# Kernel optimization log

Measured on AMD Instinct MI355X. Metric: run time of the kernel, lower is better.

## Reference

```python
import jax, jax.numpy as jnp
import numpy as np

N = 50000       # nodes
E = 1600000     # edges (avg degree 32)
D = 128         # in = hidden = out channels
H = 4           # attention heads


def setup_inputs() -> dict:
    key = jax.random.key(0)
    ks = jax.random.split(key, 9)
    s = 1.0 / np.sqrt(D)  # ~kaiming-scale linear weights
    return {
        "x": jax.random.normal(ks[0], (N, D), jnp.float32),
        "Wk": jax.random.normal(ks[1], (D, D), jnp.float32) * s,
        "bk": jnp.zeros((D,), jnp.float32),
        "Wq": jax.random.normal(ks[2], (D, D), jnp.float32) * s,
        "bq": jnp.zeros((D,), jnp.float32),
        "Wv": jax.random.normal(ks[3], (D, D), jnp.float32) * s,
        "bv": jnp.zeros((D,), jnp.float32),
        "src": jax.random.randint(ks[4], (E,), 0, N, dtype=jnp.int32),
        "dst": jax.random.randint(ks[5], (E,), 0, N, dtype=jnp.int32),
    }


def reference(x, Wk, bk, Wq, bq, Wv, bv, src, dst):
    n = x.shape[0]
    heads = H
    dk = Wk.shape[0] // heads
    dv = Wv.shape[0] // heads
    # Dense projections (near-roofline GEMMs)
    k = (x @ Wk.T + bk).reshape(n, heads, dk)
    q = (x @ Wq.T + bq).reshape(n, heads, dk)
    v = (x @ Wv.T + bv).reshape(n, heads, dv)
    # u_dot_v: per-edge per-head dot product (NO 1/sqrt(dk) scaling in source)
    scores = jnp.einsum('ehd,ehd->eh', k[src], q[dst])  # [E,H]
    # edge_softmax: softmax over incoming edges of each destination node
    m = jax.ops.segment_max(scores, dst, num_segments=n)        # [N,H]
    p = jnp.exp(scores - m[dst])                                 # [E,H]
    denom = jax.ops.segment_sum(p, dst, num_segments=n)         # [N,H]
    alpha = p / denom[dst]                                       # [E,H]
    # u_mul_e + sum: weighted scatter-aggregation of source values
    res = jax.ops.segment_sum(v[src] * alpha[:, :, None], dst, num_segments=n)  # [N,H,dv]
    # original: view(batch_size, -1, out_channels) with batch_size = N -> [N,1,out]
    return res.reshape(n, 1, heads * dv)
```

## Files before the change

kernel.cpp:

```cpp
#include <hip/hip_runtime.h>
#include <hip/hip_bf16.h>
#include <hip/hip_fp16.h>

#define NN 50000
#define NE 1600000
#define DD 128
#define HH 4
#define BSH2 5
#define NBKT2 1563
#define NBP2 2048
#define CAP 1408
#define PCHUNK 8192
#define NPB 196
#define GEMMB 782
#define MIDB (GEMMB + NPB)

typedef __attribute__((ext_vector_type(8))) short short8;
typedef __attribute__((ext_vector_type(4))) float floatx4;
typedef __attribute__((ext_vector_type(2))) _Float16 h2;

__device__ inline h2 as_h2(unsigned u) {
    union { unsigned u; h2 h; } c; c.u = u; return c.h;
}

__device__ inline float dot4(h2 a01, h2 a23, h2 b01, h2 b23) {
#if defined(__has_builtin) && __has_builtin(__builtin_amdgcn_fdot2)
    return __builtin_amdgcn_fdot2(a01, b01, __builtin_amdgcn_fdot2(a23, b23, 0.f, false), false);
#else
    return (float)a01.x * (float)b01.x + (float)a01.y * (float)b01.y +
           (float)a23.x * (float)b23.x + (float)a23.y * (float)b23.y;
#endif
}

__global__ __launch_bounds__(256) void prep_w(
    const float* __restrict__ Wk, const float* __restrict__ Wq, const float* __restrict__ Wv,
    unsigned short* __restrict__ hi, unsigned short* __restrict__ lo, int* __restrict__ bcur)
{
    int j = blockIdx.x * 256 + threadIdx.x;
    if (j < NBP2) bcur[j] = 0;
    if (j >= 3 * DD * DD) return;
    int which = j / (DD * DD);
    int off = j - which * (DD * DD);
    const float* W = (which == 0) ? Wk : (which == 1) ? Wq : Wv;
    float w = W[off];
    unsigned int b = __float_as_uint(w);
    unsigned short h = (unsigned short)(b >> 16);
    float hf = __uint_as_float((unsigned int)h << 16);
    float l = w - hf;
    hi[j] = h;
    lo[j] = (unsigned short)(__float_as_uint(l) >> 16);
}

__global__ __launch_bounds__(256) void mid(
    const float* __restrict__ x,
    const unsigned short* __restrict__ whi, const unsigned short* __restrict__ wlo,
    const float* __restrict__ bk, const float* __restrict__ bq, const float* __restrict__ bv,
    uint4* __restrict__ kvpack, __half* __restrict__ qh,
    const int* __restrict__ src, const int* __restrict__ dst,
    int* __restrict__ bcur, int* __restrict__ epack)
{
    __shared__ __align__(16) unsigned char smem[32768];

    if (blockIdx.x < GEMMB) {
        unsigned short (*stage)[4096] = (unsigned short (*)[4096])smem;
        int wave = threadIdx.x >> 6;
        int tile = blockIdx.x * 4 + wave;
        int n0 = tile * 16;
        if (n0 >= NN) return;
        int lane = threadIdx.x & 63;
        int m    = lane & 15;
        int quad = lane >> 4;

        const float* xrow = x + (size_t)(n0 + m) * DD + quad * 8;
        short8 ah[4], al[4];
#pragma unroll
        for (int ks = 0; ks < 4; ++ks) {
            const float* xr = xrow + ks * 32;
            float4 t0 = *(const float4*)xr;
            float4 t1 = *(const float4*)(xr + 4);
            float xv[8] = {t0.x, t0.y, t0.z, t0.w, t1.x, t1.y, t1.z, t1.w};
#pragma unroll
            for (int j = 0; j < 8; ++j) {
                unsigned int b = __float_as_uint(xv[j]);
                unsigned short h = (unsigned short)(b >> 16);
                float hf = __uint_as_float((unsigned int)h << 16);
                float l = xv[j] - hf;
                ah[ks][j] = (short)h;
                al[ks][j] = (short)(__float_as_uint(l) >> 16);
            }
        }

        floatx4 acc[3][8];
#pragma unroll
        for (int p = 0; p < 3; ++p)
#pragma unroll
            for (int ct = 0; ct < 8; ++ct)
                acc[p][ct] = (floatx4){0.f, 0.f, 0.f, 0.f};

#pragma unroll
        for (int ks = 0; ks < 4; ++ks) {
#pragma unroll
            for (int p = 0; p < 3; ++p) {
                size_t base = (size_t)p * DD * DD + (size_t)m * DD + ks * 32 + quad * 8;
#pragma unroll
                for (int ct = 0; ct < 8; ++ct) {
                    size_t o = base + (size_t)ct * 16 * DD;
                    short8 bh = *(const short8*)(whi + o);
                    short8 bl = *(const short8*)(wlo + o);
                    acc[p][ct] = __builtin_amdgcn_mfma_f32_16x16x32_bf16(ah[ks], bh, acc[p][ct], 0, 0, 0);
                    acc[p][ct] = __builtin_amdgcn_mfma_f32_16x16x32_bf16(ah[ks], bl, acc[p][ct], 0, 0, 0);
                    acc[p][ct] = __builtin_amdgcn_mfma_f32_16x16x32_bf16(al[ks], bh, acc[p][ct], 0, 0, 0);
                }
            }
        }

        int col = lane & 15;
        unsigned short* st = stage[wave];
        uint4* st4 = (uint4*)st;

#pragma unroll
        for (int ct = 0; ct < 8; ++ct) {
            int j = ct * 16 + col;
            int g = j >> 2, slot = j & 3;
            float biask = bk[j], biasv = bv[j];
#pragma unroll
            for (int r = 0; r < 4; ++r) {
                int row = quad * 4 + r;
                st[row * 256 + g * 8 + slot]     = __half_as_ushort(__float2half(acc[0][ct][r] + biask));
                st[row * 256 + g * 8 + 4 + slot] = __half_as_ushort(__float2half(acc[2][ct][r] + biasv));
            }
        }
#pragma unroll
        for (int t = 0; t < 8; ++t) {
            int flat = t * 64 + lane;
            kvpack[((size_t)n0 + (flat >> 5)) * 32 + (flat & 31)] = st4[flat];
        }

#pragma unroll
        for (int ct = 0; ct < 8; ++ct) {
            int j = ct * 16 + col;
            float biasq = bq[j];
#pragma unroll
            for (int r = 0; r < 4; ++r) {
                int row = quad * 4 + r;
                st[row * 128 + j] = __half_as_ushort(__float2half(acc[1][ct][r] + biasq));
            }
        }
#pragma unroll
        for (int t = 0; t < 4; ++t) {
            int flat = t * 64 + lane;
            ((uint4*)qh)[((size_t)n0 + (flat >> 4)) * 16 + (flat & 15)] = st4[flat];
        }
    } else {
        int* h  = (int*)smem;
        int* c2 = h + NBP2;
        int pb = blockIdx.x - GEMMB;
        int b0 = pb * PCHUNK;
        int n = min(PCHUNK, NE - b0);
        for (int i = threadIdx.x; i < NBP2; i += 256) h[i] = 0;
        __syncthreads();
        for (int i = threadIdx.x; i < n; i += 256)
            atomicAdd(&h[dst[b0 + i] >> BSH2], 1);
        __syncthreads();
        for (int i = threadIdx.x; i < NBP2; i += 256)
            c2[i] = h[i] ? i * CAP + atomicAdd(&bcur[i], h[i]) : 0;
        __syncthreads();
        for (int i = threadIdx.x; i < n; i += 256) {
            int d = dst[b0 + i];
            int s = src[b0 + i];
            int bkt = d >> BSH2;
            int pos = atomicAdd(&c2[bkt], 1);
            if (pos < (bkt + 1) * CAP)
                epack[pos] = ((d & 31) << 16) | s;
        }
    }
}

__global__ __launch_bounds__(256) void gat_bucket(
    const __half* __restrict__ qh, const uint4* __restrict__ kvpack,
    const int* __restrict__ epack, const int* __restrict__ bcur,
    float* __restrict__ out)
{
    __shared__ int hist[32];
    __shared__ int cur[32];
    __shared__ int begs[33];
    __shared__ unsigned short els[CAP];
    int b = blockIdx.x;
    int cnt = min(bcur[b], CAP);
    int base = b * CAP;
    int n0 = b << BSH2;
    int nnodes = min(32, NN - n0);
    int tid = threadIdx.x;

    if (tid < 32) hist[tid] = 0;
    __syncthreads();
    for (int e = tid; e < cnt; e += 256)
        atomicAdd(&hist[epack[base + e] >> 16], 1);
    __syncthreads();
    if (tid < 32) {
        int c = hist[tid], inc = c;
#pragma unroll
        for (int d = 1; d < 32; d <<= 1) {
            int t = __shfl_up(inc, d);
            if (tid >= d) inc += t;
        }
        int excl = inc - c;
        begs[tid] = excl;
        cur[tid]  = excl;
        if (tid == 31) begs[32] = excl + c;
    }
    __syncthreads();
    for (int e = tid; e < cnt; e += 256) {
        int p = epack[base + e];
        int pos = atomicAdd(&cur[p >> 16], 1);
        els[pos] = (unsigned short)(p & 0xFFFF);
    }
    __syncthreads();

    int il = tid & 31;
    int hw = tid >> 5;

    for (int nl = hw; nl < nnodes; nl += 8) {
        int node = n0 + nl;
        int beg = begs[nl], end = begs[nl + 1];

        uint2 qq = *(const uint2*)(qh + (size_t)node * 128 + il * 4);
        h2 qh01 = as_h2(qq.x), qh23 = as_h2(qq.y);

        float m = -INFINITY, ssum = 0.f;
        float o0 = 0.f, o1 = 0.f, o2 = 0.f, o3 = 0.f;

        for (int j = beg; j < end; j += 8) {
            int nh = min(8, end - j);
            uint4 kvv[8];
#pragma unroll
            for (int i = 0; i < 8; ++i) {
                int s = els[j + ((i < nh) ? i : 0)];
                kvv[i] = kvpack[(size_t)s * 32 + il];
            }
            float p[8];
#pragma unroll
            for (int i = 0; i < 8; ++i) {
                float t = dot4(as_h2(kvv[i].x), as_h2(kvv[i].y), qh01, qh23);
                t += __shfl_xor(t, 1);
                t += __shfl_xor(t, 2);
                t += __shfl_xor(t, 4);
                p[i] = (i < nh) ? t : -INFINITY;
            }
            float gm = fmaxf(fmaxf(fmaxf(p[0], p[1]), fmaxf(p[2], p[3])),
                             fmaxf(fmaxf(p[4], p[5]), fmaxf(p[6], p[7])));
            float nm = fmaxf(m, gm);
            float nmc = fmaxf(nm, -1e30f);
            float scale = __expf(m - nmc);
            ssum *= scale; o0 *= scale; o1 *= scale; o2 *= scale; o3 *= scale;
#pragma unroll
            for (int i = 0; i < 8; ++i) {
                float w = __expf(p[i] - nmc);
                ssum += w;
                o0 += w * (float)as_h2(kvv[i].z).x;
                o1 += w * (float)as_h2(kvv[i].z).y;
                o2 += w * (float)as_h2(kvv[i].w).x;
                o3 += w * (float)as_h2(kvv[i].w).y;
            }
            m = nm;
        }

        float invd = (ssum > 0.f) ? 1.f / ssum : 0.f;
        float4 r = {o0 * invd, o1 * invd, o2 * invd, o3 * invd};
        *(float4*)(out + (size_t)node * DD + il * 4) = r;
    }
}

extern "C" void kernel_launch(void* const* d_in, const int* in_sizes, int n_in,
                              void* d_out, int out_size, void* d_ws, size_t ws_size,
                              hipStream_t stream) {
    const float* x  = (const float*)d_in[0];
    const float* Wk = (const float*)d_in[1];
    const float* bk = (const float*)d_in[2];
    const float* Wq = (const float*)d_in[3];
    const float* bq = (const float*)d_in[4];
    const float* Wv = (const float*)d_in[5];
    const float* bv = (const float*)d_in[6];
    const int* src = (const int*)d_in[7];
    const int* dst = (const int*)d_in[8];

    uint4*  kvpack = (uint4*)d_ws;
    __half* qh     = (__half*)(kvpack + (size_t)NN * 32);
    unsigned short* whi = (unsigned short*)(qh + (size_t)NN * DD);
    unsigned short* wlo = whi + (size_t)3 * DD * DD;
    int* epack = (int*)(wlo + (size_t)3 * DD * DD);
    int* bcur  = epack + (size_t)NBKT2 * CAP;

    prep_w<<<(3 * DD * DD + 255) / 256, 256, 0, stream>>>(Wk, Wq, Wv, whi, wlo, bcur);
    mid<<<MIDB, 256, 0, stream>>>(x, whi, wlo, bk, bq, bv, kvpack, qh, src, dst, bcur, epack);
    gat_bucket<<<NBKT2, 256, 0, stream>>>(qh, kvpack, epack, bcur, (float*)d_out);
}
```

Baseline: 304.8 us.

## Split fused GEMM/partition kernel and double-buffer KV gathers in attention

The combined kernel that ran the QKV GEMM and the edge bucketing side by side is split into two separate launches. The partition now uses smaller chunks over more blocks to spread the shared-memory histogram work. In the per-bucket attention kernel, the KV gathers for the next group of 8 edges are issued before the current group is computed, using two register buffers to hide gather latency. The cost is one extra kernel launch, the lost overlap between GEMM and partition, more global atomics on bcur from the extra blocks, and higher register pressure.

```diff
diff --git a/kernel.cpp b/kernel.cpp
--- a/kernel.cpp
+++ b/kernel.cpp
@@ -10,10 +10,9 @@
 #define NBKT2 1563
 #define NBP2 2048
 #define CAP 1408
-#define PCHUNK 8192
-#define NPB 196
+#define PCHUNK 2048
+#define NPB 782
 #define GEMMB 782
-#define MIDB (GEMMB + NPB)
 
 typedef __attribute__((ext_vector_type(8))) short short8;
 typedef __attribute__((ext_vector_type(4))) float floatx4;
@@ -51,128 +50,126 @@
     lo[j] = (unsigned short)(__float_as_uint(l) >> 16);
 }
 
-__global__ __launch_bounds__(256) void mid(
+__global__ __launch_bounds__(256) void partition(
+    const int* __restrict__ src, const int* __restrict__ dst,
+    int* __restrict__ bcur, int* __restrict__ epack)
+{
+    __shared__ int h[NBP2];
+    __shared__ int c2[NBP2];
+    int b0 = blockIdx.x * PCHUNK;
+    int n = min(PCHUNK, NE - b0);
+    for (int i = threadIdx.x; i < NBP2; i += 256) h[i] = 0;
+    __syncthreads();
+    for (int i = threadIdx.x; i < n; i += 256)
+        atomicAdd(&h[dst[b0 + i] >> BSH2], 1);
+    __syncthreads();
+    for (int i = threadIdx.x; i < NBP2; i += 256)
+        c2[i] = h[i] ? i * CAP + atomicAdd(&bcur[i], h[i]) : 0;
+    __syncthreads();
+    for (int i = threadIdx.x; i < n; i += 256) {
+        int d = dst[b0 + i];
+        int s = src[b0 + i];
+        int bkt = d >> BSH2;
+        int pos = atomicAdd(&c2[bkt], 1);
+        if (pos < (bkt + 1) * CAP)
+            epack[pos] = ((d & 31) << 16) | s;
+    }
+}
+
+__global__ __launch_bounds__(256) void gemm_qkv(
     const float* __restrict__ x,
     const unsigned short* __restrict__ whi, const unsigned short* __restrict__ wlo,
     const float* __restrict__ bk, const float* __restrict__ bq, const float* __restrict__ bv,
-    uint4* __restrict__ kvpack, __half* __restrict__ qh,
-    const int* __restrict__ src, const int* __restrict__ dst,
-    int* __restrict__ bcur, int* __restrict__ epack)
+    uint4* __restrict__ kvpack, __half* __restrict__ qh)
 {
-    __shared__ __align__(16) unsigned char smem[32768];
-
-    if (blockIdx.x < GEMMB) {
-        unsigned short (*stage)[4096] = (unsigned short (*)[4096])smem;
-        int wave = threadIdx.x >> 6;
-        int tile = blockIdx.x * 4 + wave;
-        int n0 = tile * 16;
-        if (n0 >= NN) return;
-        int lane = threadIdx.x & 63;
-        int m    = lane & 15;
-        int quad = lane >> 4;
-
-        const float* xrow = x + (size_t)(n0 + m) * DD + quad * 8;
-        short8 ah[4], al[4];
-#pragma unroll
-        for (int ks = 0; ks < 4; ++ks) {
-            const float* xr = xrow + ks * 32;
-            float4 t0 = *(const float4*)xr;
-            float4 t1 = *(const float4*)(xr + 4);
-            float xv[8] = {t0.x, t0.y, t0.z, t0.w, t1.x, t1.y, t1.z, t1.w};
-#pragma unroll
-            for (int j = 0; j < 8; ++j) {
-                unsigned int b = __float_as_uint(xv[j]);
-                unsigned short h = (unsigned short)(b >> 16);
-                float hf = __uint_as_float((unsigned int)h << 16);
-                float l = xv[j] - hf;
-                ah[ks][j] = (short)h;
-                al[ks][j] = (short)(__float_as_uint(l) >> 16);
-            }
-        }
-
-        floatx4 acc[3][8];
-#pragma unroll
-        for (int p = 0; p < 3; ++p)
-#pragma unroll
-            for (int ct = 0; ct < 8; ++ct)
-                acc[p][ct] = (floatx4){0.f, 0.f, 0.f, 0.f};
-
-#pragma unroll
-        for (int ks = 0; ks < 4; ++ks) {
-#pragma unroll
-            for (int p = 0; p < 3; ++p) {
-                size_t base = (size_t)p * DD * DD + (size_t)m * DD + ks * 32 + quad * 8;
-#pragma unroll
-                for (int ct = 0; ct < 8; ++ct) {
-                    size_t o = base + (size_t)ct * 16 * DD;
-                    short8 bh = *(const short8*)(whi + o);
-                    short8 bl = *(const short8*)(wlo + o);
-                    acc[p][ct] = __builtin_amdgcn_mfma_f32_16x16x32_bf16(ah[ks], bh, acc[p][ct], 0, 0, 0);
-                    acc[p][ct] = __builtin_amdgcn_mfma_f32_16x16x32_bf16(ah[ks], bl, acc[p][ct], 0, 0, 0);
-                    acc[p][ct] = __builtin_amdgcn_mfma_f32_16x16x32_bf16(al[ks], bh, acc[p][ct], 0, 0, 0);
-                }
-            }
-        }
-
-        int col = lane & 15;
-        unsigned short* st = stage[wave];
-        uint4* st4 = (uint4*)st;
-
-#pragma unroll
-        for (int ct = 0; ct < 8; ++ct) {
-            int j = ct * 16 + col;
-            int g = j >> 2, slot = j & 3;
-            float biask = bk[j], biasv = bv[j];
-#pragma unroll
-            for (int r = 0; r < 4; ++r) {
-                int row = quad * 4 + r;
-                st[row * 256 + g * 8 + slot]     = __half_as_ushort(__float2half(acc[0][ct][r] + biask));
-                st[row * 256 + g * 8 + 4 + slot] = __half_as_ushort(__float2half(acc[2][ct][r] + biasv));
-            }
-        }
-#pragma unroll
-        for (int t = 0; t < 8; ++t) {
-            int flat = t * 64 + lane;
-            kvpack[((size_t)n0 + (flat >> 5)) * 32 + (flat & 31)] = st4[flat];
-        }
-
-#pragma unroll
-        for (int ct = 0; ct < 8; ++ct) {
-            int j = ct * 16 + col;
-            float biasq = bq[j];
-#pragma unroll
-            for (int r = 0; r < 4; ++r) {
-                int row = quad * 4 + r;
-                st[row * 128 + j] = __half_as_ushort(__float2half(acc[1][ct][r] + biasq));
-            }
-        }
-#pragma unroll
-        for (int t = 0; t < 4; ++t) {
-            int flat = t * 64 + lane;
-            ((uint4*)qh)[((size_t)n0 + (flat >> 4)) * 16 + (flat & 15)] = st4[flat];
-        }
-    } else {
-        int* h  = (int*)smem;
-        int* c2 = h + NBP2;
-        int pb = blockIdx.x - GEMMB;
-        int b0 = pb * PCHUNK;
-        int n = min(PCHUNK, NE - b0);
-        for (int i = threadIdx.x; i < NBP2; i += 256) h[i] = 0;
-        __syncthreads();
-        for (int i = threadIdx.x; i < n; i += 256)
-            atomicAdd(&h[dst[b0 + i] >> BSH2], 1);
-        __syncthreads();
-        for (int i = threadIdx.x; i < NBP2; i += 256)
-            c2[i] = h[i] ? i * CAP + atomicAdd(&bcur[i], h[i]) : 0;
-        __syncthreads();
-        for (int i = threadIdx.x; i < n; i += 256) {
-            int d = dst[b0 + i];
-            int s = src[b0 + i];
-            int bkt = d >> BSH2;
-            int pos = atomicAdd(&c2[bkt], 1);
-            if (pos < (bkt + 1) * CAP)
-                epack[pos] = ((d & 31) << 16) | s;
-        }
+    __shared__ __align__(16) unsigned short stage[4][4096];
+    int wave = threadIdx.x >> 6;
+    int tile = blockIdx.x * 4 + wave;
+    int n0 = tile * 16;
+    if (n0 >= NN) return;
+    int lane = threadIdx.x & 63;
+    int m    = lane & 15;
+    int quad = lane >> 4;
+
+    const float* xrow = x + (size_t)(n0 + m) * DD + quad * 8;
+    short8 ah[4], al[4];
+#pragma unroll
+    for (int ks = 0; ks < 4; ++ks) {
+        const float* xr = xrow + ks * 32;
+        float4 t0 = *(const float4*)xr;
+        float4 t1 = *(const float4*)(xr + 4);
+        float xv[8] = {t0.x, t0.y, t0.z, t0.w, t1.x, t1.y, t1.z, t1.w};
+#pragma unroll
+        for (int j = 0; j < 8; ++j) {
+            unsigned int b = __float_as_uint(xv[j]);
+            unsigned short h = (unsigned short)(b >> 16);
+            float hf = __uint_as_float((unsigned int)h << 16);
+            float l = xv[j] - hf;
+            ah[ks][j] = (short)h;
+            al[ks][j] = (short)(__float_as_uint(l) >> 16);
+        }
+    }
+
+    floatx4 acc[3][8];
+#pragma unroll
+    for (int p = 0; p < 3; ++p)
+#pragma unroll
+        for (int ct = 0; ct < 8; ++ct)
+            acc[p][ct] = (floatx4){0.f, 0.f, 0.f, 0.f};
+
+#pragma unroll
+    for (int ks = 0; ks < 4; ++ks) {
+#pragma unroll
+        for (int p = 0; p < 3; ++p) {
+            size_t base = (size_t)p * DD * DD + (size_t)m * DD + ks * 32 + quad * 8;
+#pragma unroll
+            for (int ct = 0; ct < 8; ++ct) {
+                size_t o = base + (size_t)ct * 16 * DD;
+                short8 bh = *(const short8*)(whi + o);
+                short8 bl = *(const short8*)(wlo + o);
+                acc[p][ct] = __builtin_amdgcn_mfma_f32_16x16x32_bf16(ah[ks], bh, acc[p][ct], 0, 0, 0);
+                acc[p][ct] = __builtin_amdgcn_mfma_f32_16x16x32_bf16(ah[ks], bl, acc[p][ct], 0, 0, 0);
+                acc[p][ct] = __builtin_amdgcn_mfma_f32_16x16x32_bf16(al[ks], bh, acc[p][ct], 0, 0, 0);
+            }
+        }
+    }
+
+    int col = lane & 15;
+    unsigned short* st = stage[wave];
+    uint4* st4 = (uint4*)st;
+
+#pragma unroll
+    for (int ct = 0; ct < 8; ++ct) {
+        int j = ct * 16 + col;
+        int g = j >> 2, slot = j & 3;
+        float biask = bk[j], biasv = bv[j];
+#pragma unroll
+        for (int r = 0; r < 4; ++r) {
+            int row = quad * 4 + r;
+            st[row * 256 + g * 8 + slot]     = __half_as_ushort(__float2half(acc[0][ct][r] + biask));
+            st[row * 256 + g * 8 + 4 + slot] = __half_as_ushort(__float2half(acc[2][ct][r] + biasv));
+        }
+    }
+#pragma unroll
+    for (int t = 0; t < 8; ++t) {
+        int flat = t * 64 + lane;
+        kvpack[((size_t)n0 + (flat >> 5)) * 32 + (flat & 31)] = st4[flat];
+    }
+
+#pragma unroll
+    for (int ct = 0; ct < 8; ++ct) {
+        int j = ct * 16 + col;
+        float biasq = bq[j];
+#pragma unroll
+        for (int r = 0; r < 4; ++r) {
+            int row = quad * 4 + r;
+            st[row * 128 + j] = __half_as_ushort(__float2half(acc[1][ct][r] + biasq));
+        }
+    }
+#pragma unroll
+    for (int t = 0; t < 4; ++t) {
+        int flat = t * 64 + lane;
+        ((uint4*)qh)[((size_t)n0 + (flat >> 4)) * 16 + (flat & 15)] = st4[flat];
     }
 }
 
@@ -230,18 +227,22 @@
         float m = -INFINITY, ssum = 0.f;
         float o0 = 0.f, o1 = 0.f, o2 = 0.f, o3 = 0.f;
 
-        for (int j = beg; j < end; j += 8) {
+        uint4 kva[8], kvb[8];
+
+        auto loadb = [&](uint4* kv, int j) {
             int nh = min(8, end - j);
-            uint4 kvv[8];
 #pragma unroll
             for (int i = 0; i < 8; ++i) {
                 int s = els[j + ((i < nh) ? i : 0)];
-                kvv[i] = kvpack[(size_t)s * 32 + il];
-            }
+                kv[i] = kvpack[(size_t)s * 32 + il];
+            }
+        };
+        auto computeb = [&](const uint4* kv, int j) {
+            int nh = min(8, end - j);
             float p[8];
 #pragma unroll
             for (int i = 0; i < 8; ++i) {
-                float t = dot4(as_h2(kvv[i].x), as_h2(kvv[i].y), qh01, qh23);
+                float t = dot4(as_h2(kv[i].x), as_h2(kv[i].y), qh01, qh23);
                 t += __shfl_xor(t, 1);
                 t += __shfl_xor(t, 2);
                 t += __shfl_xor(t, 4);
@@ -257,12 +258,29 @@
             for (int i = 0; i < 8; ++i) {
                 float w = __expf(p[i] - nmc);
                 ssum += w;
-                o0 += w * (float)as_h2(kvv[i].z).x;
-                o1 += w * (float)as_h2(kvv[i].z).y;
-                o2 += w * (float)as_h2(kvv[i].w).x;
-                o3 += w * (float)as_h2(kvv[i].w).y;
+                o0 += w * (float)as_h2(kv[i].z).x;
+                o1 += w * (float)as_h2(kv[i].z).y;
+                o2 += w * (float)as_h2(kv[i].w).x;
+                o3 += w * (float)as_h2(kv[i].w).y;
             }
             m = nm;
+        };
+
+        if (beg < end) {
+            int j = beg;
+            loadb(kva, j);
+            for (;;) {
+                int jn = j + 8;
+                if (jn < end) loadb(kvb, jn);
+                computeb(kva, j);
+                j = jn;
+                if (j >= end) break;
+                jn = j + 8;
+                if (jn < end) loadb(kva, jn);
+                computeb(kvb, j);
+                j = jn;
+                if (j >= end) break;
+            }
         }
 
         float invd = (ssum > 0.f) ? 1.f / ssum : 0.f;
@@ -292,6 +310,7 @@
     int* bcur  = epack + (size_t)NBKT2 * CAP;
 
     prep_w<<<(3 * DD * DD + 255) / 256, 256, 0, stream>>>(Wk, Wq, Wv, whi, wlo, bcur);
-    mid<<<MIDB, 256, 0, stream>>>(x, whi, wlo, bk, bq, bv, kvpack, qh, src, dst, bcur, epack);
+    partition<<<NPB, 256, 0, stream>>>(src, dst, bcur, epack);
+    gemm_qkv<<<GEMMB, 256, 0, stream>>>(x, whi, wlo, bk, bq, bv, kvpack, qh);
     gat_bucket<<<NBKT2, 256, 0, stream>>>(qh, kvpack, epack, bcur, (float*)d_out);
 }
```

Result: slower. 349.4 us (+14.7%).
